# Optimization experiments

Hardware: AMD Instinct MI355X
Metric: run time of the kernel (lower is better)

## Reference

```python
import jax, jax.numpy as jnp
import numpy as np

N = 50000   # nodes
E = 800000  # edges (no self-loops; self-loops added in forward)
B = 128     # graphs
EPS = 1e-16  # PyG softmax denominator epsilon


def _gat(x, W, a_src, a_dst, bias, src, dst, heads, C, concat):
    n = x.shape[0]
    xp = (x @ W).reshape(n, heads, C)                      # [N,H,C]
    s_src = (xp * a_src).sum(-1)                           # [N,H]
    s_dst = (xp * a_dst).sum(-1)                           # [N,H]
    alpha = jax.nn.leaky_relu(s_src[src] + s_dst[dst], 0.2)  # [E',H]
    m = jax.ops.segment_max(alpha, dst, num_segments=n)
    ex = jnp.exp(alpha - m[dst])
    den = jax.ops.segment_sum(ex, dst, num_segments=n) + EPS
    a = ex / den[dst]                                      # edge softmax over in-edges
    out = jax.ops.segment_sum(a[:, :, None] * xp[src], dst, num_segments=n)  # [N,H,C]
    out = out.reshape(n, heads * C) if concat else out.mean(axis=1)
    return out + bias


def _forward(x, edge_attr, W1, b1, ln_g, ln_b, W2, b2,
             Wg1, as1, ad1, bg1, Wg2, as2, ad2, bg2, Wg3, as3, ad3, bg3,
             Wih, Whh, bih, bhh, edge_index, batch):
    # feature encoder: Linear -> LayerNorm -> LeakyReLU(0.1) -> Linear (dropout: eval mode)
    h = x @ W1 + b1
    mu = h.mean(-1, keepdims=True)
    var = ((h - mu) ** 2).mean(-1, keepdims=True)
    h = (h - mu) / jnp.sqrt(var + 1e-5) * ln_g + ln_b
    h = jax.nn.leaky_relu(h, 0.1)
    h = h @ W2 + b2                                        # [N,256]
    # add self loops once (edge_attr is unused: edge_dim=None => lin_edge is None)
    sl = jnp.arange(N, dtype=edge_index.dtype)
    src = jnp.concatenate([edge_index[0], sl])
    dst = jnp.concatenate([edge_index[1], sl])
    g = _gat(h, Wg1, as1, ad1, bg1, src, dst, 2, 64, True)   # [N,128]
    g = jax.nn.leaky_relu(g, 0.1)
    g = _gat(g, Wg2, as2, ad2, bg2, src, dst, 2, 64, True)   # [N,128]
    g = jax.nn.elu(g)
    g = _gat(g, Wg3, as3, ad3, bg3, src, dst, 1, 64, False)  # [N,64]
    # Set2Set(64, processing_steps=5)
    q_star = jnp.zeros((B, 128), g.dtype)
    hS = jnp.zeros((B, 64), g.dtype)
    cS = jnp.zeros((B, 64), g.dtype)
    for _ in range(5):
        gates = q_star @ Wih.T + bih + hS @ Whh.T + bhh      # [B,256]
        i, f, gg, o = jnp.split(gates, 4, axis=-1)
        cS = jax.nn.sigmoid(f) * cS + jax.nn.sigmoid(i) * jnp.tanh(gg)
        hS = jax.nn.sigmoid(o) * jnp.tanh(cS)                # q = h [B,64]
        e = (g * hS[batch]).sum(-1)                          # [N]
        m = jax.ops.segment_max(e, batch, num_segments=B)
        a = jnp.exp(e - m[batch])
        a = a / (jax.ops.segment_sum(a, batch, num_segments=B) + EPS)[batch]
        r = jax.ops.segment_sum(a[:, None] * g, batch, num_segments=B)  # [B,64]
        q_star = jnp.concatenate([hS, r], axis=-1)
    return q_star  # [B,128]


def setup_inputs():
    key = jax.random.key(0)
    ks = jax.random.split(key, 32)
    nrm = lambda k, sh, s=0.1: (jax.random.normal(k, sh) * s).astype(jnp.float32)
    src = jax.random.randint(ks[0], (E,), 0, N, dtype=jnp.int32)
    off = jax.random.randint(ks[1], (E,), 1, N, dtype=jnp.int32)
    dst = (src + off) % N  # no self-loops
    edge_index = jnp.stack([src, dst])
    batch = jnp.sort(jax.random.randint(ks[2], (N,), 0, B, dtype=jnp.int32))
    return dict(
        x=jax.random.normal(ks[3], (N, 6), jnp.float32),
        edge_index=edge_index,
        edge_attr=jax.random.normal(ks[4], (E, 4), jnp.float32),
        batch=batch,
        W1=nrm(ks[5], (6, 128)), b1=jnp.zeros((128,), jnp.float32),
        ln_g=jnp.ones((128,), jnp.float32), ln_b=jnp.zeros((128,), jnp.float32),
        W2=nrm(ks[6], (128, 256)), b2=jnp.zeros((256,), jnp.float32),
        Wg1=nrm(ks[7], (256, 128)), as1=nrm(ks[8], (2, 64)), ad1=nrm(ks[9], (2, 64)), bg1=jnp.zeros((128,), jnp.float32),
        Wg2=nrm(ks[10], (128, 128)), as2=nrm(ks[11], (2, 64)), ad2=nrm(ks[12], (2, 64)), bg2=jnp.zeros((128,), jnp.float32),
        Wg3=nrm(ks[13], (128, 64)), as3=nrm(ks[14], (1, 64)), ad3=nrm(ks[15], (1, 64)), bg3=jnp.zeros((64,), jnp.float32),
        Wih=nrm(ks[16], (256, 128)), Whh=nrm(ks[17], (256, 64)),
        bih=jnp.zeros((256,), jnp.float32), bhh=jnp.zeros((256,), jnp.float32),
    )


def reference(x, edge_index, edge_attr, batch, W1, b1, ln_g, ln_b, W2, b2,
              Wg1, as1, ad1, bg1, Wg2, as2, ad2, bg2, Wg3, as3, ad3, bg3,
              Wih, Whh, bih, bhh):
    return _forward(x, edge_attr, W1, b1, ln_g, ln_b, W2, b2,
                    Wg1, as1, ad1, bg1, Wg2, as2, ad2, bg2, Wg3, as3, ad3, bg3,
                    Wih, Whh, bih, bhh, edge_index, batch)
```

## Files before the change

### kernel.cpp

```cpp
#include <hip/hip_runtime.h>
#include <hip/hip_bf16.h>
#include <math.h>

#define N_NODES 50000
#define M_PAD   50176
#define N_EDGES 800000
#define N_B     128
#define EPRIME  (N_EDGES + N_NODES)
#define NBUCKETS 196
#define CCHUNK  8192
#define NCHUNKS ((EPRIME + CCHUNK - 1) / CCHUNK)
#define ENC_B   ((N_NODES + 3) / 4)
#define WT_B    (90112 / 256)
#define S2S_MAXN 576

typedef __attribute__((ext_vector_type(8))) short bf16x8;
typedef __attribute__((ext_vector_type(4))) float f32x4;
typedef unsigned short ushort_t;

__device__ __forceinline__ float sigmoidf_(float x) { return 1.f / (1.f + __expf(-x)); }

__device__ __forceinline__ void wtr1(const float* W, __hip_bfloat16* Wt, int K, int N, int i) {
    int k = i / N, n = i - k * N;
    Wt[(size_t)n * K + k] = __float2bfloat16(W[i]);
}

__global__ __launch_bounds__(256) void prep_k(
        const float* __restrict__ x, const float* __restrict__ W1,
        const float* __restrict__ b1, const float* __restrict__ lng,
        const float* __restrict__ lnb, __hip_bfloat16* __restrict__ h1,
        const float* __restrict__ W2, const float* __restrict__ Wg1,
        const float* __restrict__ Wg2, const float* __restrict__ Wg3,
        __hip_bfloat16* W2t, __hip_bfloat16* Wg1t,
        __hip_bfloat16* Wg2t, __hip_bfloat16* Wg3t,
        const int* __restrict__ e_dst, int* __restrict__ bpart) {
    int blk = blockIdx.x;
    if (blk < ENC_B) {
        int w = (blk * 256 + threadIdx.x) >> 6;
        int lane = threadIdx.x & 63;
        if (w >= N_NODES) return;
        float xr[6];
#pragma unroll
        for (int k = 0; k < 6; ++k) xr[k] = x[w * 6 + k];
        float a = b1[lane], b = b1[lane + 64];
#pragma unroll
        for (int k = 0; k < 6; ++k) {
            a += xr[k] * W1[k * 128 + lane];
            b += xr[k] * W1[k * 128 + 64 + lane];
        }
        float s = a + b, s2 = a * a + b * b;
        for (int o = 32; o; o >>= 1) { s += __shfl_xor(s, o); s2 += __shfl_xor(s2, o); }
        float mu  = s * (1.f / 128.f);
        float var = s2 * (1.f / 128.f) - mu * mu;
        float inv = rsqrtf(var + 1e-5f);
        a = (a - mu) * inv * lng[lane] + lnb[lane];
        b = (b - mu) * inv * lng[lane + 64] + lnb[lane + 64];
        a = a > 0.f ? a : 0.1f * a;
        b = b > 0.f ? b : 0.1f * b;
        h1[(size_t)w * 128 + lane]      = __float2bfloat16(a);
        h1[(size_t)w * 128 + 64 + lane] = __float2bfloat16(b);
    } else if (blk < ENC_B + WT_B) {
        int i = (blk - ENC_B) * 256 + threadIdx.x;
        if (i < 32768)       wtr1(W2,  W2t,  128, 256, i);
        else if (i < 65536)  wtr1(Wg1, Wg1t, 256, 128, i - 32768);
        else if (i < 81920)  wtr1(Wg2, Wg2t, 128, 128, i - 65536);
        else                 wtr1(Wg3, Wg3t, 128, 64,  i - 81920);
    } else {
        __shared__ int h[NBUCKETS];
        int c = blk - ENC_B - WT_B;
        for (int i = threadIdx.x; i < NBUCKETS; i += 256) h[i] = 0;
        __syncthreads();
        int base = c * CCHUNK;
        int end = min(base + CCHUNK, EPRIME);
        for (int e = base + threadIdx.x; e < end; e += 256) {
            int d = (e < N_EDGES) ? e_dst[e] : (e - N_EDGES);
            atomicAdd(&h[d >> 8], 1);
        }
        __syncthreads();
        for (int i = threadIdx.x; i < NBUCKETS; i += 256)
            bpart[c * NBUCKETS + i] = h[i];
    }
}

__global__ __launch_bounds__(256) void scan2_k(const int* __restrict__ bpart,
        int* __restrict__ boff, int* __restrict__ cpre) {
    __shared__ int sm[256];
    int t = threadIdx.x;
    int run = 0;
    if (t < NBUCKETS) {
        for (int j = 0; j < NCHUNKS; ++j) {
            cpre[j * NBUCKETS + t] = run;
            run += bpart[j * NBUCKETS + t];
        }
    }
    sm[t] = run; __syncthreads();
    for (int o = 1; o < 256; o <<= 1) {
        int xv = (t >= o) ? sm[t - o] : 0;
        __syncthreads();
        sm[t] += xv;
        __syncthreads();
    }
    int excl = sm[t] - run;
    if (t < NBUCKETS) boff[t] = excl;
    if (t == NBUCKETS - 1) boff[NBUCKETS] = excl + run;
}

__global__ __launch_bounds__(256) void partition_k(const int* __restrict__ e_src,
        const int* __restrict__ e_dst, const int* __restrict__ boff,
        const int* __restrict__ cpre, int* __restrict__ epack) {
    __shared__ int h2[NBUCKETS], gbase[NBUCKETS];
    int c = blockIdx.x;
    for (int i = threadIdx.x; i < NBUCKETS; i += 256) {
        h2[i] = 0;
        gbase[i] = boff[i] + cpre[c * NBUCKETS + i];
    }
    __syncthreads();
    int base = c * CCHUNK;
    int end = min(base + CCHUNK, EPRIME);
    for (int e = base + threadIdx.x; e < end; e += 256) {
        int s, d;
        if (e < N_EDGES) { s = e_src[e]; d = e_dst[e]; }
        else             { s = e - N_EDGES; d = s; }
        int b = d >> 8;
        int rank = atomicAdd(&h2[b], 1);
        epack[gbase[b] + rank] = ((d & 255) << 16) | s;
    }
}

__global__ __launch_bounds__(256) void csr_build_k(const int* __restrict__ epack,
        const int* __restrict__ boff, int* __restrict__ off,
        ushort_t* __restrict__ csr) {
    __shared__ int deg[256], cur[256], sm[256];
    int b = blockIdx.x, t = threadIdx.x;
    int gb0 = boff[b];
    int gcnt = boff[b + 1] - gb0;
    deg[t] = 0;
    __syncthreads();
    for (int i = t; i < gcnt; i += 256)
        atomicAdd(&deg[(epack[gb0 + i] >> 16) & 0xFF], 1);
    __syncthreads();
    int v = deg[t];
    sm[t] = v; __syncthreads();
    for (int o = 1; o < 256; o <<= 1) {
        int xv = (t >= o) ? sm[t - o] : 0;
        __syncthreads();
        sm[t] += xv;
        __syncthreads();
    }
    int excl = sm[t] - v;
    int idx = b * 256 + t;
    if (idx <= N_NODES) off[idx] = gb0 + excl;
    cur[t] = gb0 + excl;
    __syncthreads();
    for (int i = t; i < gcnt; i += 256) {
        int pk = epack[gb0 + i];
        int ld = (pk >> 16) & 0xFF;
        int pos = atomicAdd(&cur[ld], 1);
        csr[pos] = (ushort_t)(pk & 0xFFFF);
    }
}

template<int K, int N, int BM, int BN, int WM, int WN, bool BIAS, int SDH>
__global__ __launch_bounds__(256) void mfma_gemm_k(
        const __hip_bfloat16* __restrict__ A,
        const __hip_bfloat16* __restrict__ Wt,
        const float* __restrict__ bias, void* __restrict__ Cv,
        const float* __restrict__ asrc, const float* __restrict__ adst,
        float* __restrict__ ssrc, float* __restrict__ sdst, int M) {
    constexpr int KT = K / 32;
    constexpr int NISSUE = BM / 64;
    __shared__ short As[BM * 32];
    __shared__ float sdbuf[SDH > 0 ? BM * SDH * 2 : 1];
    const int tid  = threadIdx.x;
    const int wid  = tid >> 6;
    const int lane = tid & 63;
    const int wm = wid / WN;
    const int wn = wid % WN;
    const int row0 = blockIdx.y * BM;
    const int col0 = blockIdx.x * BN + wn * 32;

    if (SDH > 0) {
        for (int i = tid; i < BM * SDH * 2; i += 256) sdbuf[i] = 0.f;
    }

    bf16x8 breg[KT][2];
#pragma unroll
    for (int kt = 0; kt < KT; ++kt)
#pragma unroll
        for (int cb = 0; cb < 2; ++cb) {
            int col = col0 + cb * 16 + (lane & 15);
            int k   = kt * 32 + (lane >> 4) * 8;
            breg[kt][cb] = *(const bf16x8*)&Wt[(size_t)col * K + k];
        }

    f32x4 acc[4][2];
#pragma unroll
    for (int rb = 0; rb < 4; ++rb)
#pragma unroll
        for (int cb = 0; cb < 2; ++cb) acc[rb][cb] = f32x4{0.f, 0.f, 0.f, 0.f};

    int4 rbuf[NISSUE];
#pragma unroll
    for (int is = 0; is < NISSUE; ++is) {
        int lr = is * 64 + wid * 16 + (lane >> 2);
        rbuf[is] = *(const int4*)&A[(size_t)(row0 + lr) * K + (lane & 3) * 8];
    }
#pragma unroll
    for (int kt = 0; kt < KT; ++kt) {
        if (kt) __syncthreads();
#pragma unroll
        for (int is = 0; is < NISSUE; ++is) {
            int lr   = is * 64 + wid * 16 + (lane >> 2);
            int slot = (lane & 3) ^ ((lr >> 1) & 3);
            *(int4*)((char*)As + lr * 64 + slot * 16) = rbuf[is];
        }
        if (kt + 1 < KT) {
#pragma unroll
            for (int is = 0; is < NISSUE; ++is) {
                int lr = is * 64 + wid * 16 + (lane >> 2);
                rbuf[is] = *(const int4*)&A[(size_t)(row0 + lr) * K +
                                            (kt + 1) * 32 + (lane & 3) * 8];
            }
        }
        __syncthreads();
        bf16x8 af[4];
#pragma unroll
        for (int rb = 0; rb < 4; ++rb) {
            int row  = wm * 64 + rb * 16 + (lane & 15);
            int slot = (lane >> 4) ^ ((row >> 1) & 3);
            af[rb] = *(const bf16x8*)((char*)As + row * 64 + slot * 16);
        }
#pragma unroll
        for (int rb = 0; rb < 4; ++rb)
#pragma unroll
            for (int cb = 0; cb < 2; ++cb)
                acc[rb][cb] = __builtin_amdgcn_mfma_f32_16x16x32_bf16(
                    af[rb], breg[kt][cb], acc[rb][cb], 0, 0, 0);
    }

    if (SDH > 0) {
        float av0 = asrc[col0 + (lane & 15)],       ad0 = adst[col0 + (lane & 15)];
        float av1 = asrc[col0 + 16 + (lane & 15)],  ad1 = adst[col0 + 16 + (lane & 15)];
        int h = (SDH == 2) ? (wn >> 1) : 0;
#pragma unroll
        for (int rb = 0; rb < 4; ++rb) {
#pragma unroll
            for (int r = 0; r < 4; ++r) {
                float ssv = acc[rb][0][r] * av0 + acc[rb][1][r] * av1;
                float sdv = acc[rb][0][r] * ad0 + acc[rb][1][r] * ad1;
#pragma unroll
                for (int o = 1; o < 16; o <<= 1) {
                    ssv += __shfl_xor(ssv, o);
                    sdv += __shfl_xor(sdv, o);
                }
                if ((lane & 15) == 0) {
                    int rl = wm * 64 + rb * 16 + (lane >> 4) * 4 + r;
                    atomicAdd(&sdbuf[(rl * SDH + h) * 2 + 0], ssv);
                    atomicAdd(&sdbuf[(rl * SDH + h) * 2 + 1], sdv);
                }
            }
        }
        __syncthreads();
        if (tid < BM) {
            int row = row0 + tid;
            if (row < M) {
                if (SDH == 2) {
                    ((float2*)ssrc)[row] = make_float2(sdbuf[(tid * 2 + 0) * 2 + 0],
                                                       sdbuf[(tid * 2 + 1) * 2 + 0]);
                    ((float2*)sdst)[row] = make_float2(sdbuf[(tid * 2 + 0) * 2 + 1],
                                                       sdbuf[(tid * 2 + 1) * 2 + 1]);
                } else {
                    ssrc[row] = sdbuf[tid * 2 + 0];
                    sdst[row] = sdbuf[tid * 2 + 1];
                }
            }
        }
    }

#pragma unroll
    for (int rb = 0; rb < 4; ++rb) {
        int rowb = row0 + wm * 64 + rb * 16 + (lane >> 4) * 4;
#pragma unroll
        for (int cb = 0; cb < 2; ++cb) {
            int col = col0 + cb * 16 + (lane & 15);
            float bval = BIAS ? bias[col] : 0.f;
#pragma unroll
            for (int r = 0; r < 4; ++r) {
                int row = rowb + r;
                if (row < M) {
                    float v = acc[rb][cb][r] + bval;
                    ((__hip_bfloat16*)Cv)[(size_t)row * N + col] = __float2bfloat16(v);
                }
            }
        }
    }
}

template<int ACT>
__global__ __launch_bounds__(256) void gat_agg2_k(const __hip_bfloat16* __restrict__ xp,
        const float2* __restrict__ s_src2, const float2* __restrict__ s_dst2,
        const int* __restrict__ off, const ushort_t* __restrict__ csr_src,
        const float* __restrict__ bias, __hip_bfloat16* __restrict__ outb) {
    int n = (blockIdx.x * 256 + threadIdx.x) >> 6;
    int lane = threadIdx.x & 63;
    if (n >= N_NODES) return;
    const float2 sdn = s_dst2[n];
    const int i0 = off[n];
    const int deg = off[n + 1] - i0;
    const unsigned* __restrict__ xprow = (const unsigned*)xp;
    float accx = 0.f, accy = 0.f;
    float d0 = 0.f, d1 = 0.f;
    for (int c0 = 0; c0 < deg; c0 += 64) {
        int cnt = min(64, deg - c0);
        int se = 0; float e0 = 0.f, e1 = 0.f;
        if (lane < cnt) {
            se = csr_src[i0 + c0 + lane];
            float2 ssv = s_src2[se];
            float a0 = ssv.x + sdn.x; a0 = a0 > 0.f ? a0 : 0.2f * a0;
            float a1 = ssv.y + sdn.y; a1 = a1 > 0.f ? a1 : 0.2f * a1;
            e0 = __expf(a0); e1 = __expf(a1);
        }
        d0 += e0; d1 += e1;
        unsigned e0u = __float_as_uint(e0), e1u = __float_as_uint(e1);
        int e = 0;
        for (; e + 4 <= cnt; e += 4) {
            int s0 = __builtin_amdgcn_readlane(se, e + 0);
            int s1 = __builtin_amdgcn_readlane(se, e + 1);
            int s2 = __builtin_amdgcn_readlane(se, e + 2);
            int s3 = __builtin_amdgcn_readlane(se, e + 3);
            unsigned w0 = xprow[((unsigned)s0 << 6) + lane];
            unsigned w1 = xprow[((unsigned)s1 << 6) + lane];
            unsigned w2 = xprow[((unsigned)s2 << 6) + lane];
            unsigned w3 = xprow[((unsigned)s3 << 6) + lane];
            float p00 = __uint_as_float(__builtin_amdgcn_readlane(e0u, e + 0));
            float p01 = __uint_as_float(__builtin_amdgcn_readlane(e1u, e + 0));
            float p10 = __uint_as_float(__builtin_amdgcn_readlane(e0u, e + 1));
            float p11 = __uint_as_float(__builtin_amdgcn_readlane(e1u, e + 1));
            float p20 = __uint_as_float(__builtin_amdgcn_readlane(e0u, e + 2));
            float p21 = __uint_as_float(__builtin_amdgcn_readlane(e1u, e + 2));
            float p30 = __uint_as_float(__builtin_amdgcn_readlane(e0u, e + 3));
            float p31 = __uint_as_float(__builtin_amdgcn_readlane(e1u, e + 3));
            float q0 = lane < 32 ? p00 : p01;
            float q1 = lane < 32 ? p10 : p11;
            float q2 = lane < 32 ? p20 : p21;
            float q3 = lane < 32 ? p30 : p31;
            accx += q0 * __uint_as_float(w0 << 16);
            accy += q0 * __uint_as_float(w0 & 0xffff0000u);
            accx += q1 * __uint_as_float(w1 << 16);
            accy += q1 * __uint_as_float(w1 & 0xffff0000u);
            accx += q2 * __uint_as_float(w2 << 16);
            accy += q2 * __uint_as_float(w2 & 0xffff0000u);
            accx += q3 * __uint_as_float(w3 << 16);
            accy += q3 * __uint_as_float(w3 & 0xffff0000u);
        }
        for (; e < cnt; ++e) {
            int s = __builtin_amdgcn_readlane(se, e);
            unsigned w = xprow[((unsigned)s << 6) + lane];
            float p0 = __uint_as_float(__builtin_amdgcn_readlane(e0u, e));
            float p1 = __uint_as_float(__builtin_amdgcn_readlane(e1u, e));
            float q = lane < 32 ? p0 : p1;
            accx += q * __uint_as_float(w << 16);
            accy += q * __uint_as_float(w & 0xffff0000u);
        }
    }
    for (int o = 32; o; o >>= 1) { d0 += __shfl_xor(d0, o); d1 += __shfl_xor(d1, o); }
    float den = (lane < 32 ? d0 : d1) + 1e-16f;
    float2 bv = ((const float2*)bias)[lane];
    float r0 = accx / den + bv.x;
    float r1 = accy / den + bv.y;
    if (ACT == 1) { r0 = r0 > 0.f ? r0 : 0.1f * r0; r1 = r1 > 0.f ? r1 : 0.1f * r1; }
    else          { r0 = r0 > 0.f ? r0 : (__expf(r0) - 1.f);
                    r1 = r1 > 0.f ? r1 : (__expf(r1) - 1.f); }
    __hip_bfloat16 h0 = __float2bfloat16(r0), h1v = __float2bfloat16(r1);
    unsigned packed = (unsigned)*(unsigned short*)&h0 |
                      ((unsigned)*(unsigned short*)&h1v << 16);
    ((unsigned*)outb)[(size_t)n * 64 + lane] = packed;
}

__global__ __launch_bounds__(256) void gat_agg1_k(const __hip_bfloat16* __restrict__ xp,
        const float* __restrict__ s_src, const float* __restrict__ s_dst,
        const int* __restrict__ off, const ushort_t* __restrict__ csr_src,
        const float* __restrict__ bias, float* __restrict__ out) {
    int n = (blockIdx.x * 256 + threadIdx.x) >> 6;
    int lane = threadIdx.x & 63;
    if (n >= N_NODES) return;
    const float sdn = s_dst[n];
    const int i0 = off[n];
    const int deg = off[n + 1] - i0;
    float acc = 0.f, d0 = 0.f;
    for (int c0 = 0; c0 < deg; c0 += 64) {
        int cnt = min(64, deg - c0);
        int se = 0; float ev = 0.f;
        if (lane < cnt) {
            se = csr_src[i0 + c0 + lane];
            float a = s_src[se] + sdn;
            a = a > 0.f ? a : 0.2f * a;
            ev = __expf(a);
        }
        d0 += ev;
        unsigned evu = __float_as_uint(ev);
        int e = 0;
        for (; e + 4 <= cnt; e += 4) {
            int s0 = __builtin_amdgcn_readlane(se, e + 0);
            int s1 = __builtin_amdgcn_readlane(se, e + 1);
            int s2 = __builtin_amdgcn_readlane(se, e + 2);
            int s3 = __builtin_amdgcn_readlane(se, e + 3);
            float w0 = __uint_as_float(__builtin_amdgcn_readlane(evu, e + 0));
            float w1 = __uint_as_float(__builtin_amdgcn_readlane(evu, e + 1));
            float w2 = __uint_as_float(__builtin_amdgcn_readlane(evu, e + 2));
            float w3 = __uint_as_float(__builtin_amdgcn_readlane(evu, e + 3));
            acc += w0 * __bfloat162float(xp[((unsigned)s0 << 6) + lane]);
            acc += w1 * __bfloat162float(xp[((unsigned)s1 << 6) + lane]);
            acc += w2 * __bfloat162float(xp[((unsigned)s2 << 6) + lane]);
            acc += w3 * __bfloat162float(xp[((unsigned)s3 << 6) + lane]);
        }
        for (; e < cnt; ++e) {
            int s = __builtin_amdgcn_readlane(se, e);
            float w = __uint_as_float(__builtin_amdgcn_readlane(evu, e));
            acc += w * __bfloat162float(xp[((unsigned)s << 6) + lane]);
        }
    }
    for (int o = 32; o; o >>= 1) d0 += __shfl_xor(d0, o);
    out[(size_t)n * 64 + lane] = acc / (d0 + 1e-16f) + bias[lane];
}

__global__ __launch_bounds__(512) void s2s_fused_k(const float* __restrict__ g3,
        const int* __restrict__ batch,
        const float* __restrict__ Wih, const float* __restrict__ Whh,
        const float* __restrict__ bih, const float* __restrict__ bhh,
        float* __restrict__ out) {
    __shared__ float g3L[S2S_MAXN * 65];
    __shared__ float p_sh[S2S_MAXN];
    __shared__ float q[128], hsh[64], csh[64], gates[256];
    __shared__ float rred[8][64];
    __shared__ float dred[8];
    __shared__ int sn0, sn1;
    int b = blockIdx.x;
    int t = threadIdx.x;
    int lane = t & 63, wv = t >> 6;
    if (t == 0) {
        int lo = 0, hi = N_NODES;
        while (lo < hi) { int mid = (lo + hi) >> 1; if (batch[mid] < b) lo = mid + 1; else hi = mid; }
        sn0 = lo;
        lo = 0; hi = N_NODES;
        while (lo < hi) { int mid = (lo + hi) >> 1; if (batch[mid] < b + 1) lo = mid + 1; else hi = mid; }
        sn1 = lo;
    }
    if (t < 128) q[t] = 0.f;
    if (t < 64) { hsh[t] = 0.f; csh[t] = 0.f; }
    __syncthreads();
    const int n0 = sn0;
    const int cnt = min(sn1 - sn0, S2S_MAXN);
    for (int i = t; i < cnt * 64; i += 512) {
        int r = i >> 6, c = i & 63;
        g3L[r * 65 + c] = g3[((size_t)(n0 + r) << 6) + c];
    }
    __syncthreads();
    for (int step = 0; step < 5; ++step) {
        if (t < 256) {
            float g = bih[t] + bhh[t];
            const float4* wi4 = (const float4*)(Wih + (size_t)t * 128);
#pragma unroll 8
            for (int k4 = 0; k4 < 32; ++k4) {
                float4 w = wi4[k4];
                g += q[k4 * 4 + 0] * w.x + q[k4 * 4 + 1] * w.y +
                     q[k4 * 4 + 2] * w.z + q[k4 * 4 + 3] * w.w;
            }
            const float4* wh4 = (const float4*)(Whh + (size_t)t * 64);
#pragma unroll 8
            for (int k4 = 0; k4 < 16; ++k4) {
                float4 w = wh4[k4];
                g += hsh[k4 * 4 + 0] * w.x + hsh[k4 * 4 + 1] * w.y +
                     hsh[k4 * 4 + 2] * w.z + hsh[k4 * 4 + 3] * w.w;
            }
            gates[t] = g;
        }
        __syncthreads();
        if (t < 64) {
            float iv = sigmoidf_(gates[t]);
            float fv = sigmoidf_(gates[64 + t]);
            float gv = tanhf(gates[128 + t]);
            float ov = sigmoidf_(gates[192 + t]);
            float c = fv * csh[t] + iv * gv;
            csh[t] = c;
            hsh[t] = ov * tanhf(c);
        }
        __syncthreads();
        for (int base = 0; base < cnt; base += 512) {
            int n = base + t;
            if (n < cnt) {
                const float* row = &g3L[n * 65];
                float dot = 0.f;
#pragma unroll 8
                for (int c = 0; c < 64; ++c) dot += row[c] * hsh[c];
                p_sh[n] = __expf(dot);
            }
        }
        __syncthreads();
        float rloc = 0.f, dloc = 0.f;
        for (int n = wv; n < cnt; n += 8) {
            float pv = p_sh[n];
            float gv = g3L[n * 65 + lane];
            dloc += pv;
            rloc += pv * gv;
        }
        rred[wv][lane] = rloc;
        if (lane == 0) dred[wv] = dloc;
        __syncthreads();
        if (t < 64) {
            float r = rred[0][t] + rred[1][t] + rred[2][t] + rred[3][t] +
                      rred[4][t] + rred[5][t] + rred[6][t] + rred[7][t];
            float den = dred[0] + dred[1] + dred[2] + dred[3] +
                        dred[4] + dred[5] + dred[6] + dred[7] + 1e-16f;
            q[t] = hsh[t];
            q[64 + t] = r / den;
        }
        __syncthreads();
    }
    if (t < 128) out[b * 128 + t] = q[t];
}

extern "C" void kernel_launch(void* const* d_in, const int* in_sizes, int n_in,
                              void* d_out, int out_size, void* d_ws, size_t ws_size,
                              hipStream_t stream) {
    (void)in_sizes; (void)n_in; (void)out_size; (void)ws_size;
    const float* x     = (const float*)d_in[0];
    const int*   ei    = (const int*)d_in[1];
    const int*   batch = (const int*)d_in[3];
    const float* W1  = (const float*)d_in[4];
    const float* b1  = (const float*)d_in[5];
    const float* lng = (const float*)d_in[6];
    const float* lnb = (const float*)d_in[7];
    const float* W2  = (const float*)d_in[8];
    const float* b2  = (const float*)d_in[9];
    const float* Wg1 = (const float*)d_in[10];
    const float* as1 = (const float*)d_in[11];
    const float* ad1 = (const float*)d_in[12];
    const float* bg1 = (const float*)d_in[13];
    const float* Wg2 = (const float*)d_in[14];
    const float* as2 = (const float*)d_in[15];
    const float* ad2 = (const float*)d_in[16];
    const float* bg2 = (const float*)d_in[17];
    const float* Wg3 = (const float*)d_in[18];
    const float* as3 = (const float*)d_in[19];
    const float* ad3 = (const float*)d_in[20];
    const float* bg3 = (const float*)d_in[21];
    const float* Wih = (const float*)d_in[22];
    const float* Whh = (const float*)d_in[23];
    const float* bih = (const float*)d_in[24];
    const float* bhh = (const float*)d_in[25];
    const int* e_src = ei;
    const int* e_dst = ei + N_EDGES;
    float* out = (float*)d_out;

    char* p = (char*)d_ws;
    auto carve = [&](size_t bytes) {
        char* r = p;
        p += (bytes + 255) & ~(size_t)255;
        return r;
    };
    __hip_bfloat16* actA = (__hip_bfloat16*)carve((size_t)M_PAD * 256 * 2);
    __hip_bfloat16* actB = (__hip_bfloat16*)carve((size_t)M_PAD * 128 * 2);
    __hip_bfloat16* actC = (__hip_bfloat16*)carve((size_t)M_PAD * 128 * 2);
    float* g3     = (float*)carve((size_t)M_PAD * 64 * 4);
    float* s_src  = (float*)carve((size_t)N_NODES * 2 * 4);
    float* s_dst  = (float*)carve((size_t)N_NODES * 2 * 4);
    int*   off    = (int*)carve((size_t)(N_NODES + 1) * 4);
    int*   epack  = (int*)carve((size_t)EPRIME * 4);
    ushort_t* csr = (ushort_t*)carve((size_t)EPRIME * 2);
    int*   bpart  = (int*)carve((size_t)NCHUNKS * NBUCKETS * 4);
    int*   cpre   = (int*)carve((size_t)NCHUNKS * NBUCKETS * 4);
    int*   boff   = (int*)carve((NBUCKETS + 1) * 4);
    __hip_bfloat16* W2t  = (__hip_bfloat16*)carve(256 * 128 * 2);
    __hip_bfloat16* Wg1t = (__hip_bfloat16*)carve(128 * 256 * 2);
    __hip_bfloat16* Wg2t = (__hip_bfloat16*)carve(128 * 128 * 2);
    __hip_bfloat16* Wg3t = (__hip_bfloat16*)carve(64 * 128 * 2);

    dim3 blk(256);

    prep_k<<<ENC_B + WT_B + NCHUNKS, blk, 0, stream>>>(
        x, W1, b1, lng, lnb, actB,
        W2, Wg1, Wg2, Wg3, W2t, Wg1t, Wg2t, Wg3t,
        e_dst, bpart);

    scan2_k<<<1, blk, 0, stream>>>(bpart, boff, cpre);
    partition_k<<<NCHUNKS, blk, 0, stream>>>(e_src, e_dst, boff, cpre, epack);
    csr_build_k<<<NBUCKETS, blk, 0, stream>>>(epack, boff, off, csr);

    mfma_gemm_k<128, 256, 64, 128, 1, 4, true, 0>
        <<<dim3(2, 782), blk, 0, stream>>>(actB, W2t, b2, actA,
                                           nullptr, nullptr, nullptr, nullptr, N_NODES);

    mfma_gemm_k<256, 128, 64, 128, 1, 4, false, 2>
        <<<dim3(1, 782), blk, 0, stream>>>(actA, Wg1t, nullptr, actB,
                                           as1, ad1, s_src, s_dst, N_NODES);
    gat_agg2_k<1><<<(N_NODES + 3) / 4, blk, 0, stream>>>(
        actB, (const float2*)s_src, (const float2*)s_dst, off, csr, bg1, actC);

    mfma_gemm_k<128, 128, 64, 128, 1, 4, false, 2>
        <<<dim3(1, 782), blk, 0, stream>>>(actC, Wg2t, nullptr, actB,
                                           as2, ad2, s_src, s_dst, N_NODES);
    gat_agg2_k<2><<<(N_NODES + 3) / 4, blk, 0, stream>>>(
        actB, (const float2*)s_src, (const float2*)s_dst, off, csr, bg2, actC);

    mfma_gemm_k<128, 64, 128, 64, 2, 2, false, 1>
        <<<dim3(1, 391), blk, 0, stream>>>(actC, Wg3t, nullptr, actB,
                                           as3, ad3, s_src, s_dst, N_NODES);
    gat_agg1_k<<<(N_NODES + 3) / 4, blk, 0, stream>>>(
        actB, s_src, s_dst, off, csr, bg3, g3);

    s2s_fused_k<<<N_B, dim3(512), 0, stream>>>(g3, batch, Wih, Whh, bih, bhh, out);
}
```

Measured before the change: 423.0 us.

## Co-schedule edge partition and CSR build with encoder GEMMs; vectorize Set2Set

```diff
diff --git a/kernel.cpp b/kernel.cpp
--- a/kernel.cpp
+++ b/kernel.cpp
@@ -12,7 +12,9 @@
 #define NCHUNKS ((EPRIME + CCHUNK - 1) / CCHUNK)
 #define ENC_B   ((N_NODES + 3) / 4)
 #define WT_B    (90112 / 256)
-#define S2S_MAXN 576
+#define S2S_MAXN 512
+#define GEMME_B  1564
+#define GEMM1_B  782
 
 typedef __attribute__((ext_vector_type(8))) short bf16x8;
 typedef __attribute__((ext_vector_type(4))) float f32x4;
@@ -105,11 +107,10 @@
     if (t == NBUCKETS - 1) boff[NBUCKETS] = excl + run;
 }
 
-__global__ __launch_bounds__(256) void partition_k(const int* __restrict__ e_src,
+__device__ __forceinline__ void partition_body(int c, const int* __restrict__ e_src,
         const int* __restrict__ e_dst, const int* __restrict__ boff,
-        const int* __restrict__ cpre, int* __restrict__ epack) {
-    __shared__ int h2[NBUCKETS], gbase[NBUCKETS];
-    int c = blockIdx.x;
+        const int* __restrict__ cpre, int* __restrict__ epack,
+        int* h2, int* gbase) {
     for (int i = threadIdx.x; i < NBUCKETS; i += 256) {
         h2[i] = 0;
         gbase[i] = boff[i] + cpre[c * NBUCKETS + i];
@@ -127,11 +128,10 @@
     }
 }
 
-__global__ __launch_bounds__(256) void csr_build_k(const int* __restrict__ epack,
+__device__ __forceinline__ void csr_build_body(int b, const int* __restrict__ epack,
         const int* __restrict__ boff, int* __restrict__ off,
-        ushort_t* __restrict__ csr) {
-    __shared__ int deg[256], cur[256], sm[256];
-    int b = blockIdx.x, t = threadIdx.x;
+        ushort_t* __restrict__ csr, int* deg, int* cur, int* sm) {
+    int t = threadIdx.x;
     int gb0 = boff[b];
     int gcnt = boff[b + 1] - gb0;
     deg[t] = 0;
@@ -160,24 +160,21 @@
     }
 }
 
-template<int K, int N, int BM, int BN, int WM, int WN, bool BIAS, int SDH>
-__global__ __launch_bounds__(256) void mfma_gemm_k(
-        const __hip_bfloat16* __restrict__ A,
-        const __hip_bfloat16* __restrict__ Wt,
+template<int K, int N, int BM, int BN, int WN, bool BIAS, int SDH>
+__device__ __forceinline__ void mfma_body(short* As, float* sdbuf, int bx, int by,
+        const __hip_bfloat16* __restrict__ A, const __hip_bfloat16* __restrict__ Wt,
         const float* __restrict__ bias, void* __restrict__ Cv,
         const float* __restrict__ asrc, const float* __restrict__ adst,
         float* __restrict__ ssrc, float* __restrict__ sdst, int M) {
     constexpr int KT = K / 32;
     constexpr int NISSUE = BM / 64;
-    __shared__ short As[BM * 32];
-    __shared__ float sdbuf[SDH > 0 ? BM * SDH * 2 : 1];
     const int tid  = threadIdx.x;
     const int wid  = tid >> 6;
     const int lane = tid & 63;
     const int wm = wid / WN;
     const int wn = wid % WN;
-    const int row0 = blockIdx.y * BM;
-    const int col0 = blockIdx.x * BN + wn * 32;
+    const int row0 = by * BM;
+    const int col0 = bx * BN + wn * 32;
 
     if (SDH > 0) {
         for (int i = tid; i < BM * SDH * 2; i += 256) sdbuf[i] = 0.f;
@@ -294,6 +291,54 @@
             }
         }
     }
+}
+
+__global__ __launch_bounds__(256) void gemmE_part_k(
+        const __hip_bfloat16* __restrict__ A, const __hip_bfloat16* __restrict__ Wt,
+        const float* __restrict__ bias, __hip_bfloat16* __restrict__ C,
+        const int* __restrict__ e_src, const int* __restrict__ e_dst,
+        const int* __restrict__ boff, const int* __restrict__ cpre,
+        int* __restrict__ epack) {
+    __shared__ short As[64 * 32];
+    __shared__ int h2[NBUCKETS], gbase[NBUCKETS];
+    int blk = blockIdx.x;
+    if (blk < GEMME_B) {
+        mfma_body<128, 256, 64, 128, 4, true, 0>(As, nullptr, blk & 1, blk >> 1,
+            A, Wt, bias, C, nullptr, nullptr, nullptr, nullptr, N_NODES);
+    } else {
+        partition_body(blk - GEMME_B, e_src, e_dst, boff, cpre, epack, h2, gbase);
+    }
+}
+
+__global__ __launch_bounds__(256) void gemm1_csr_k(
+        const __hip_bfloat16* __restrict__ A, const __hip_bfloat16* __restrict__ Wt,
+        __hip_bfloat16* __restrict__ C,
+        const float* __restrict__ asrc, const float* __restrict__ adst,
+        float* __restrict__ ssrc, float* __restrict__ sdst,
+        const int* __restrict__ epack, const int* __restrict__ boff,
+        int* __restrict__ off, ushort_t* __restrict__ csr) {
+    __shared__ short As[64 * 32];
+    __shared__ float sdbuf[64 * 2 * 2];
+    __shared__ int deg[256], cur[256], sm[256];
+    int blk = blockIdx.x;
+    if (blk < GEMM1_B) {
+        mfma_body<256, 128, 64, 128, 4, false, 2>(As, sdbuf, 0, blk,
+            A, Wt, nullptr, C, asrc, adst, ssrc, sdst, N_NODES);
+    } else {
+        csr_build_body(blk - GEMM1_B, epack, boff, off, csr, deg, cur, sm);
+    }
+}
+
+template<int K, int N, int BM, int BN, int WN, int SDH>
+__global__ __launch_bounds__(256) void gemm_k(
+        const __hip_bfloat16* __restrict__ A, const __hip_bfloat16* __restrict__ Wt,
+        __hip_bfloat16* __restrict__ C,
+        const float* __restrict__ asrc, const float* __restrict__ adst,
+        float* __restrict__ ssrc, float* __restrict__ sdst) {
+    __shared__ short As[BM * 32];
+    __shared__ float sdbuf[SDH > 0 ? BM * SDH * 2 : 1];
+    mfma_body<K, N, BM, BN, WN, false, SDH>(As, sdbuf, 0, blockIdx.x,
+        A, Wt, nullptr, C, asrc, adst, ssrc, sdst, N_NODES);
 }
 
 template<int ACT>
@@ -429,9 +474,10 @@
         const float* __restrict__ Wih, const float* __restrict__ Whh,
         const float* __restrict__ bih, const float* __restrict__ bhh,
         float* __restrict__ out) {
-    __shared__ float g3L[S2S_MAXN * 65];
+    __shared__ __align__(16) float g3L[S2S_MAXN * 68];
     __shared__ float p_sh[S2S_MAXN];
-    __shared__ float q[128], hsh[64], csh[64], gates[256];
+    __shared__ __align__(16) float hsh[64];
+    __shared__ float q[128], csh[64], gates[256];
     __shared__ float rred[8][64];
     __shared__ float dred[8];
     __shared__ int sn0, sn1;
@@ -451,9 +497,9 @@
     __syncthreads();
     const int n0 = sn0;
     const int cnt = min(sn1 - sn0, S2S_MAXN);
-    for (int i = t; i < cnt * 64; i += 512) {
-        int r = i >> 6, c = i & 63;
-        g3L[r * 65 + c] = g3[((size_t)(n0 + r) << 6) + c];
+    for (int i = t; i < cnt * 16; i += 512) {
+        int r = i >> 4, c4 = i & 15;
+        ((float4*)&g3L[r * 68])[c4] = ((const float4*)(g3 + ((size_t)(n0 + r) << 6)))[c4];
     }
     __syncthreads();
     for (int step = 0; step < 5; ++step) {
@@ -486,23 +532,38 @@
             hsh[t] = ov * tanhf(c);
         }
         __syncthreads();
+        float4 hr[16];
+#pragma unroll
+        for (int k = 0; k < 16; ++k) hr[k] = ((const float4*)hsh)[k];
         for (int base = 0; base < cnt; base += 512) {
             int n = base + t;
             if (n < cnt) {
-                const float* row = &g3L[n * 65];
-                float dot = 0.f;
-#pragma unroll 8
-                for (int c = 0; c < 64; ++c) dot += row[c] * hsh[c];
-                p_sh[n] = __expf(dot);
+                const float4* row = (const float4*)&g3L[n * 68];
+                float a0 = 0.f, a1 = 0.f, a2 = 0.f, a3 = 0.f;
+#pragma unroll
+                for (int k = 0; k < 16; k += 4) {
+                    float4 r0 = row[k], r1 = row[k + 1], r2 = row[k + 2], r3 = row[k + 3];
+                    a0 += r0.x * hr[k].x + r0.y * hr[k].y + r0.z * hr[k].z + r0.w * hr[k].w;
+                    a1 += r1.x * hr[k+1].x + r1.y * hr[k+1].y + r1.z * hr[k+1].z + r1.w * hr[k+1].w;
+                    a2 += r2.x * hr[k+2].x + r2.y * hr[k+2].y + r2.z * hr[k+2].z + r2.w * hr[k+2].w;
+                    a3 += r3.x * hr[k+3].x + r3.y * hr[k+3].y + r3.z * hr[k+3].z + r3.w * hr[k+3].w;
+                }
+                p_sh[n] = __expf((a0 + a1) + (a2 + a3));
             }
         }
         __syncthreads();
         float rloc = 0.f, dloc = 0.f;
-        for (int n = wv; n < cnt; n += 8) {
+        int n = wv;
+        for (; n + 8 < cnt; n += 16) {
+            float pv0 = p_sh[n], pv1 = p_sh[n + 8];
+            float gv0 = g3L[n * 68 + lane], gv1 = g3L[(n + 8) * 68 + lane];
+            dloc += pv0 + pv1;
+            rloc += pv0 * gv0 + pv1 * gv1;
+        }
+        if (n < cnt) {
             float pv = p_sh[n];
-            float gv = g3L[n * 65 + lane];
-            dloc += pv;
-            rloc += pv * gv;
+            float gv = g3L[n * 68 + lane];
+            dloc += pv; rloc += pv * gv;
         }
         rred[wv][lane] = rloc;
         if (lane == 0) dred[wv] = dloc;
@@ -584,28 +645,22 @@
         e_dst, bpart);
 
     scan2_k<<<1, blk, 0, stream>>>(bpart, boff, cpre);
-    partition_k<<<NCHUNKS, blk, 0, stream>>>(e_src, e_dst, boff, cpre, epack);
-    csr_build_k<<<NBUCKETS, blk, 0, stream>>>(epack, boff, off, csr);
-
-    mfma_gemm_k<128, 256, 64, 128, 1, 4, true, 0>
-        <<<dim3(2, 782), blk, 0, stream>>>(actB, W2t, b2, actA,
-                                           nullptr, nullptr, nullptr, nullptr, N_NODES);
-
-    mfma_gemm_k<256, 128, 64, 128, 1, 4, false, 2>
-        <<<dim3(1, 782), blk, 0, stream>>>(actA, Wg1t, nullptr, actB,
-                                           as1, ad1, s_src, s_dst, N_NODES);
+
+    gemmE_part_k<<<GEMME_B + NCHUNKS, blk, 0, stream>>>(
+        actB, W2t, b2, actA, e_src, e_dst, boff, cpre, epack);
+
+    gemm1_csr_k<<<GEMM1_B + NBUCKETS, blk, 0, stream>>>(
+        actA, Wg1t, actB, as1, ad1, s_src, s_dst, epack, boff, off, csr);
     gat_agg2_k<1><<<(N_NODES + 3) / 4, blk, 0, stream>>>(
         actB, (const float2*)s_src, (const float2*)s_dst, off, csr, bg1, actC);
 
-    mfma_gemm_k<128, 128, 64, 128, 1, 4, false, 2>
-        <<<dim3(1, 782), blk, 0, stream>>>(actC, Wg2t, nullptr, actB,
-                                           as2, ad2, s_src, s_dst, N_NODES);
+    gemm_k<128, 128, 64, 128, 4, 2><<<GEMM1_B, blk, 0, stream>>>(
+        actC, Wg2t, actB, as2, ad2, s_src, s_dst);
     gat_agg2_k<2><<<(N_NODES + 3) / 4, blk, 0, stream>>>(
         actB, (const float2*)s_src, (const float2*)s_dst, off, csr, bg2, actC);
 
-    mfma_gemm_k<128, 64, 128, 64, 2, 2, false, 1>
-        <<<dim3(1, 391), blk, 0, stream>>>(actC, Wg3t, nullptr, actB,
-                                           as3, ad3, s_src, s_dst, N_NODES);
+    gemm_k<128, 64, 128, 64, 2, 1><<<391, blk, 0, stream>>>(
+        actC, Wg3t, actB, as3, ad3, s_src, s_dst);
     gat_agg1_k<<<(N_NODES + 3) / 4, blk, 0, stream>>>(
         actB, s_src, s_dst, off, csr, bg3, g3);
 
```

New measurement: 398.2 us. 5.9% less time.
